# Optimization experiments

Measured on AMD Instinct MI355X. Metric: run time of the kernel, lower is better.

## Reference

```python
import jax, jax.numpy as jnp
import numpy as np

LN_EPS = 1e-5

def _layernorm(x, w, b):
    mu = jnp.mean(x, axis=-1, keepdims=True)
    var = jnp.mean((x - mu) ** 2, axis=-1, keepdims=True)
    return (x - mu) * jax.lax.rsqrt(var + LN_EPS) * w + b

def _parallel_scan(A, B, x):
    # A, B, x: (Bb, L, S). Log-space cumsum trick, faithful to torch version.
    A_safe = jnp.clip(A, 0.001, 0.999)
    log_A = jnp.log(A_safe + 1e-10)
    log_cum_A = jnp.cumsum(log_A, axis=1)
    log_cum_A_max = jnp.max(log_cum_A, axis=1, keepdims=True)
    log_cum_A_c = log_cum_A - log_cum_A_max
    cum_A = jnp.exp(log_cum_A_c)
    BX = B * x
    # shifted (exclusive) centered log-cumsum: zeros at t=0
    zeros = jnp.zeros_like(log_cum_A_c[:, :1])
    log_cum_shift = jnp.concatenate([zeros, log_cum_A_c[:, :-1]], axis=1)
    BX_norm = BX * jnp.exp(-log_cum_shift)
    cum_BX = jnp.cumsum(BX_norm, axis=1)
    return cum_BX * cum_A

def setup_inputs() -> dict:
    key = jax.random.key(0)
    ks = jax.random.split(key, 8)
    Bb, L, D, S = 16, 4096, 512, 64
    def xavier(k, shape, gain):
        fan_out, fan_in = shape
        std = gain * np.sqrt(2.0 / (fan_in + fan_out))
        return jax.random.normal(k, shape, jnp.float32) * std
    x = jax.random.normal(ks[0], (Bb, L, D), jnp.float32)
    Wx = xavier(ks[1], (S, D), 0.5)
    Wdt = xavier(ks[2], (S, D), 1.0)
    WB = xavier(ks[3], (S, D), 0.4)
    WC = xavier(ks[4], (S, D), 0.4)
    Wout = xavier(ks[5], (D, S), 0.5)
    # A_init = -rand*0.8 - 0.2 ; A_log = log(-A_init) = log(uniform(0.2, 1.0))
    A_log = jnp.log(jax.random.uniform(ks[6], (S,), jnp.float32, 0.2, 1.0))
    return {
        "x": x,
        "ln_w": jnp.ones((D,), jnp.float32),
        "ln_b": jnp.zeros((D,), jnp.float32),
        "Wx": Wx, "bx": jnp.zeros((S,), jnp.float32),
        "Wdt": Wdt, "bdt": jnp.zeros((S,), jnp.float32),
        "A_log": A_log,
        "WB": WB, "WC": WC,
        "Dp": jnp.zeros((D,), jnp.float32),
        "Wout": Wout, "bout": jnp.zeros((D,), jnp.float32),
    }

def reference(x, ln_w, ln_b, Wx, bx, Wdt, bdt, A_log, WB, WC, Dp, Wout, bout):
    x_norm = _layernorm(x, ln_w, ln_b)                       # (B,L,D)
    delta = jax.nn.softplus(x_norm @ Wdt.T + bdt) * 0.01 + 0.0001  # (B,L,S)
    B_t = x_norm @ WB.T                                      # (B,L,S)
    C_t = x_norm @ WC.T                                      # (B,L,S)
    A = -jnp.exp(A_log)                                      # (S,)
    x_proj = x_norm @ Wx.T + bx                              # (B,L,S)
    deltaA = jnp.clip(delta * A, -10.0, -0.0001)
    A_disc = jnp.exp(deltaA)
    B_disc = delta * B_t
    h = _parallel_scan(A_disc, B_disc, x_proj)               # (B,L,S)
    y = C_t * h
    y = jnp.where(jnp.any(~jnp.isfinite(y)), jnp.zeros_like(y), y)
    y = y @ Wout.T + bout                                    # (B,L,D)
    D_safe = jnp.clip(Dp, -2.0, 2.0)
    return y + D_safe * x
```

## Files before the change

### kernel.cpp

```cpp
#include <hip/hip_runtime.h>
#include <math.h>

typedef __attribute__((ext_vector_type(4))) float  floatx4;
typedef __attribute__((ext_vector_type(8))) short  shortx8;
typedef unsigned short ushort_t;
typedef unsigned int   uint32;

#define BB 16
#define LL 4096
#define DD 512
#define SS 64
#define NTOK (BB*LL)
#define NCH 64

__device__ __forceinline__ ushort_t f2bf(float f) {
    uint32 u = __float_as_uint(f);
    u += 0x7FFFu + ((u >> 16) & 1u);
    return (ushort_t)(u >> 16);
}

__global__ __launch_bounds__(256) void k_prep(
    const float* __restrict__ Wdt, const float* __restrict__ WB,
    const float* __restrict__ WC,  const float* __restrict__ Wx,
    const float* __restrict__ Wout,
    ushort_t* __restrict__ wcat, ushort_t* __restrict__ woutb)
{
    int tid = blockIdx.x * 256 + threadIdx.x;
    int n = tid >> 9, k = tid & 511;
    const float* src = (n < 64) ? Wdt : (n < 128) ? WB : (n < 192) ? WC : Wx;
    wcat[tid] = f2bf(src[(n & 63) * 512 + k]);
    if (tid < 512 * 64) woutb[tid] = f2bf(Wout[tid]);
}

__global__ __launch_bounds__(256) void k_ln_proj(
    const float* __restrict__ x, const float* __restrict__ lnw, const float* __restrict__ lnb,
    const ushort_t* __restrict__ wcat,
    const float* __restrict__ bdt, const float* __restrict__ bx_, const float* __restrict__ A_log,
    float* __restrict__ Ap, float* __restrict__ BXv, float* __restrict__ Ct,
    float* __restrict__ Asum, float* __restrict__ Bsum)
{
    __shared__ float sMean[64], sRstd[64];
    __shared__ __align__(16) char sBuf[46080];
    ushort_t* sA = (ushort_t*)sBuf;
    ushort_t* sB = sA + 64 * 72;
    float*    sPA = (float*)sBuf;
    float*    sPB = sPA + 64 * 17;

    const int tid  = threadIdx.x;
    const int wave = tid >> 6, lane = tid & 63;
    const int ln   = lane & 15, qd = lane >> 4;
    const int token0 = blockIdx.x * 64;

    for (int i = 0; i < 16; i++) {
        int tok = wave * 16 + i;
        const float4* xr = (const float4*)(x + (size_t)(token0 + tok) * DD);
        float4 a = xr[lane];
        float4 b = xr[64 + lane];
        float s = a.x + a.y + a.z + a.w + b.x + b.y + b.z + b.w;
        float q = a.x*a.x + a.y*a.y + a.z*a.z + a.w*a.w
                + b.x*b.x + b.y*b.y + b.z*b.z + b.w*b.w;
        #pragma unroll
        for (int off = 32; off > 0; off >>= 1) {
            s += __shfl_xor(s, off);
            q += __shfl_xor(q, off);
        }
        if (lane == 0) {
            float mu  = s * (1.0f / 512.0f);
            float var = q * (1.0f / 512.0f) - mu * mu;
            sMean[tok] = mu;
            sRstd[tok] = rsqrtf(var + 1e-5f);
        }
    }
    __syncthreads();

    floatx4 acc[4][4] = {};

    for (int kc = 0; kc < 8; kc++) {
        {
            int q = tid & 15, tr = tid >> 4;
            #pragma unroll
            for (int it = 0; it < 4; it++) {
                int tok = it * 16 + tr;
                float mu = sMean[tok], rs = sRstd[tok];
                float4 v  = *(const float4*)(x + (size_t)(token0 + tok) * DD + kc * 64 + q * 4);
                float4 w4 = *(const float4*)(lnw + kc * 64 + q * 4);
                float4 b4 = *(const float4*)(lnb + kc * 64 + q * 4);
                uint32 lo = (uint32)f2bf((v.x - mu) * rs * w4.x + b4.x)
                          | ((uint32)f2bf((v.y - mu) * rs * w4.y + b4.y) << 16);
                uint32 hi = (uint32)f2bf((v.z - mu) * rs * w4.z + b4.z)
                          | ((uint32)f2bf((v.w - mu) * rs * w4.w + b4.w) << 16);
                uint2 pk; pk.x = lo; pk.y = hi;
                *(uint2*)&sA[tok * 72 + q * 4] = pk;
            }
        }
        {
            #pragma unroll
            for (int it = 0; it < 8; it++) {
                int f = it * 256 + tid;
                int n = f >> 3, c8 = f & 7;
                uint4 v = *(const uint4*)(wcat + n * 512 + kc * 64 + c8 * 8);
                *(uint4*)&sB[n * 72 + c8 * 8] = v;
            }
        }
        __syncthreads();
        #pragma unroll
        for (int ks = 0; ks < 64; ks += 32) {
            shortx8 af[4], bf[4];
            #pragma unroll
            for (int mt = 0; mt < 4; mt++)
                af[mt] = *(const shortx8*)&sA[(mt * 16 + ln) * 72 + ks + qd * 8];
            #pragma unroll
            for (int nt = 0; nt < 4; nt++)
                bf[nt] = *(const shortx8*)&sB[(nt * 64 + wave * 16 + ln) * 72 + ks + qd * 8];
            #pragma unroll
            for (int mt = 0; mt < 4; mt++)
                #pragma unroll
                for (int nt = 0; nt < 4; nt++)
                    acc[mt][nt] = __builtin_amdgcn_mfma_f32_16x16x32_bf16(
                        af[mt], bf[nt], acc[mt][nt], 0, 0, 0);
        }
        __syncthreads();
    }

    {
        int s = wave * 16 + ln;
        float bdt_s = bdt[s], bx_s = bx_[s];
        float A_s = -expf(A_log[s]);
        bool fc = ((blockIdx.x & 63) == 0);
        #pragma unroll
        for (int mt = 0; mt < 4; mt++) {
            float Al = 1.f, Bl = 0.f;
            #pragma unroll
            for (int r = 0; r < 4; r++) {
                int tok = mt * 16 + qd * 4 + r;
                float zdt = acc[mt][0][r];
                float zb  = acc[mt][1][r];
                float zc  = acc[mt][2][r];
                float zx  = acc[mt][3][r];
                float zin = zdt + bdt_s;
                float sp  = fmaxf(zin, 0.0f) + log1pf(expf(-fabsf(zin)));
                float delta = sp * 0.01f + 1e-4f;
                float dA    = fminf(fmaxf(delta * A_s, -10.0f), -1e-4f);
                float Adisc = expf(dA);
                float a     = fminf(fmaxf(Adisc, 0.001f), 0.999f) + 1e-10f;
                float bxv   = delta * zb * (zx + bx_s);
                size_t g = (size_t)(token0 + tok) * 64 + s;
                Ap[g] = a; BXv[g] = bxv; Ct[g] = zc;
                bool first = fc && (tok == 0);
                float alpha = first ? 0.f : a;
                float beta  = first ? bxv : a * bxv;
                Al *= alpha;
                Bl = fmaf(alpha, Bl, beta);
            }
            sPA[s * 17 + mt * 4 + qd] = Al;
            sPB[s * 17 + mt * 4 + qd] = Bl;
        }
    }
    __syncthreads();
    if (tid < 64) {
        float A = sPA[tid * 17 + 0], B = sPB[tid * 17 + 0];
        #pragma unroll
        for (int g = 1; g < 16; g++) {
            float pa = sPA[tid * 17 + g], pb = sPB[tid * 17 + g];
            A *= pa;
            B = fmaf(pa, B, pb);
        }
        int o = blockIdx.x * 64 + tid;
        Asum[o] = A; Bsum[o] = B;
    }
}

__global__ __launch_bounds__(64) void k_scan_b(
    const float* __restrict__ Asum, const float* __restrict__ Bsum, float* __restrict__ Hin)
{
    int b = blockIdx.x, s = threadIdx.x;
    float h = 0.f;
    for (int tile = 0; tile < 4; tile++) {
        float rA[16], rB[16];
        #pragma unroll
        for (int cc = 0; cc < 16; cc++) {
            int o = (b * NCH + tile * 16 + cc) * 64 + s;
            rA[cc] = Asum[o]; rB[cc] = Bsum[o];
        }
        #pragma unroll
        for (int cc = 0; cc < 16; cc++) {
            int o = (b * NCH + tile * 16 + cc) * 64 + s;
            Hin[o] = h;
            h = fmaf(rA[cc], h, rB[cc]);
        }
    }
}

__global__ __launch_bounds__(512, 4) void k_out2(
    const float* __restrict__ Ap, const float* __restrict__ BXv, const float* __restrict__ Ct,
    const float* __restrict__ Hin, const ushort_t* __restrict__ woutb,
    const float* __restrict__ bout, const float* __restrict__ Dp,
    const float* __restrict__ x, float* __restrict__ out)
{
    __shared__ __align__(16) char buf[33024];
    ushort_t* sP   = (ushort_t*)buf;
    float*    sSA  = (float*)(buf + 9216);
    float*    sSB  = (float*)(buf + 9216 + 2048);
    float*    sOut = (float*)buf;

    const int tid  = threadIdx.x;
    const int wave = tid >> 6, lane = tid & 63;
    const int ln   = lane & 15, qd = lane >> 4;
    const int blk  = blockIdx.x;
    const int token0 = blk * 64;
    const bool fc = ((blk & 63) == 0);

    {
        const int s = lane, j = wave;
        size_t gbase = (size_t)token0 * 64 + (size_t)j * 8 * 64 + s;
        float av[8], vv[8];
        #pragma unroll
        for (int i = 0; i < 8; i++) {
            av[i] = Ap[gbase + (size_t)i * 64];
            vv[i] = BXv[gbase + (size_t)i * 64];
        }
        float Al = 1.f, Bl = 0.f;
        #pragma unroll
        for (int i = 0; i < 8; i++) {
            bool first = fc && (j == 0) && (i == 0);
            float alpha = first ? 0.f : av[i];
            float beta  = first ? vv[i] : av[i] * vv[i];
            Al *= alpha;
            Bl = fmaf(alpha, Bl, beta);
        }
        sSA[j * 64 + s] = Al;
        sSB[j * 64 + s] = Bl;
        __syncthreads();
        float h = Hin[blk * 64 + s];
        for (int jj = 0; jj < j; jj++)
            h = fmaf(sSA[jj * 64 + s], h, sSB[jj * 64 + s]);
        #pragma unroll
        for (int i = 0; i < 8; i++) {
            bool first = fc && (j == 0) && (i == 0);
            float alpha = first ? 0.f : av[i];
            float beta  = first ? vv[i] : av[i] * vv[i];
            h = fmaf(alpha, h, beta);
            float ct = Ct[gbase + (size_t)i * 64];
            sP[(j * 8 + i) * 72 + s] = f2bf(ct * h);
        }
    }
    __syncthreads();

    floatx4 acc[4][4] = {};
    const int d0 = wave * 64;
    #pragma unroll
    for (int ks = 0; ks < 64; ks += 32) {
        shortx8 af[4], bf[4];
        #pragma unroll
        for (int mt = 0; mt < 4; mt++)
            af[mt] = *(const shortx8*)&sP[(mt * 16 + ln) * 72 + ks + qd * 8];
        #pragma unroll
        for (int nt = 0; nt < 4; nt++)
            bf[nt] = *(const shortx8*)(woutb + (size_t)(d0 + nt * 16 + ln) * 64 + ks + qd * 8);
        #pragma unroll
        for (int mt = 0; mt < 4; mt++)
            #pragma unroll
            for (int nt = 0; nt < 4; nt++)
                acc[mt][nt] = __builtin_amdgcn_mfma_f32_16x16x32_bf16(
                    af[mt], bf[nt], acc[mt][nt], 0, 0, 0);
    }

    for (int mt = 0; mt < 4; mt++) {
        __syncthreads();
        #pragma unroll
        for (int nt = 0; nt < 4; nt++)
            #pragma unroll
            for (int r = 0; r < 4; r++)
                sOut[(qd * 4 + r) * 516 + d0 + nt * 16 + ln] = acc[mt][nt][r];
        __syncthreads();
        #pragma unroll
        for (int it = 0; it < 4; it++) {
            int idx = it * 512 + tid;
            int row = idx >> 7, c4 = (idx & 127) * 4;
            int tok = token0 + mt * 16 + row;
            float4 o  = *(float4*)&sOut[row * 516 + c4];
            float4 xv = *(const float4*)(x + (size_t)tok * DD + c4);
            float4 bo = *(const float4*)(bout + c4);
            float4 dp = *(const float4*)(Dp + c4);
            float4 res;
            res.x = fmaf(fminf(fmaxf(dp.x, -2.f), 2.f), xv.x, o.x + bo.x);
            res.y = fmaf(fminf(fmaxf(dp.y, -2.f), 2.f), xv.y, o.y + bo.y);
            res.z = fmaf(fminf(fmaxf(dp.z, -2.f), 2.f), xv.z, o.z + bo.z);
            res.w = fmaf(fminf(fmaxf(dp.w, -2.f), 2.f), xv.w, o.w + bo.w);
            *(float4*)(out + (size_t)tok * DD + c4) = res;
        }
    }
}

extern "C" void kernel_launch(void* const* d_in, const int* in_sizes, int n_in,
                              void* d_out, int out_size, void* d_ws, size_t ws_size,
                              hipStream_t stream)
{
    const float* x     = (const float*)d_in[0];
    const float* lnw   = (const float*)d_in[1];
    const float* lnb   = (const float*)d_in[2];
    const float* Wx    = (const float*)d_in[3];
    const float* bx_   = (const float*)d_in[4];
    const float* Wdt   = (const float*)d_in[5];
    const float* bdt   = (const float*)d_in[6];
    const float* A_log = (const float*)d_in[7];
    const float* WB    = (const float*)d_in[8];
    const float* WC    = (const float*)d_in[9];
    const float* Dp    = (const float*)d_in[10];
    const float* Wout  = (const float*)d_in[11];
    const float* bout  = (const float*)d_in[12];
    float* out = (float*)d_out;

    char* w = (char*)d_ws;
    constexpr size_t SZ_T = (size_t)NTOK * 64 * 4;
    float*    Ap    = (float*)(w);
    float*    BXv   = (float*)(w + SZ_T);
    float*    Ct    = (float*)(w + 2 * SZ_T);
    float*    Asum  = (float*)(w + 3 * SZ_T);
    float*    Bsum  = (float*)(w + 3 * SZ_T + 262144);
    float*    Hin   = (float*)(w + 3 * SZ_T + 2 * 262144);
    ushort_t* Wcat  = (ushort_t*)(w + 3 * SZ_T + 3 * 262144);
    ushort_t* WoutB = (ushort_t*)(w + 3 * SZ_T + 3 * 262144 + 262144);

    k_prep<<<512, 256, 0, stream>>>(Wdt, WB, WC, Wx, Wout, Wcat, WoutB);
    k_ln_proj<<<NTOK / 64, 256, 0, stream>>>(x, lnw, lnb, Wcat, bdt, bx_, A_log,
                                             Ap, BXv, Ct, Asum, Bsum);
    k_scan_b<<<BB, 64, 0, stream>>>(Asum, Bsum, Hin);
    k_out2<<<NTOK / 64, 512, 0, stream>>>(Ap, BXv, Ct, Hin, WoutB, bout, Dp, x, out);
}
```

Before: 341.7 us.

## Split LayerNorm into bf16 pass, use direct-to-LDS loads, restructure scan and output GEMM

LayerNorm now runs as its own kernel that writes a bf16 normalized activation buffer. The projection GEMM reads that buffer and the weights with global_load_lds into XOR-swizzled shared memory, using 128-token tiles across 8 waves. The serial per-batch scan is replaced by a wider kernel in which each block recomputes the chunk prefix from the chunk sums and writes C*h as bf16. The output GEMM is split across two blocks per token tile along D. In exchange, the normalized activations make an extra round trip through HBM and a bf16 intermediate buffer is added.

```diff
diff --git a/kernel.cpp b/kernel.cpp
--- a/kernel.cpp
+++ b/kernel.cpp
@@ -19,6 +19,12 @@
     return (ushort_t)(u >> 16);
 }
 
+__device__ __forceinline__ void gload16(const void* g, void* l) {
+    __builtin_amdgcn_global_load_lds(
+        (const __attribute__((address_space(1))) unsigned int*)g,
+        (__attribute__((address_space(3))) unsigned int*)l, 16, 0, 0);
+}
+
 __global__ __launch_bounds__(256) void k_prep(
     const float* __restrict__ Wdt, const float* __restrict__ WB,
     const float* __restrict__ WC,  const float* __restrict__ Wx,
@@ -32,86 +38,84 @@
     if (tid < 512 * 64) woutb[tid] = f2bf(Wout[tid]);
 }
 
-__global__ __launch_bounds__(256) void k_ln_proj(
+__global__ __launch_bounds__(256) void k_ln(
     const float* __restrict__ x, const float* __restrict__ lnw, const float* __restrict__ lnb,
-    const ushort_t* __restrict__ wcat,
+    ushort_t* __restrict__ xn)
+{
+    const int wave = threadIdx.x >> 6, lane = threadIdx.x & 63;
+    const int tok = blockIdx.x * 4 + wave;
+    const float4* xr = (const float4*)(x + (size_t)tok * DD);
+    float4 a = xr[lane * 2], b = xr[lane * 2 + 1];
+    float s = a.x + a.y + a.z + a.w + b.x + b.y + b.z + b.w;
+    float q = a.x*a.x + a.y*a.y + a.z*a.z + a.w*a.w
+            + b.x*b.x + b.y*b.y + b.z*b.z + b.w*b.w;
+    #pragma unroll
+    for (int off = 32; off > 0; off >>= 1) {
+        s += __shfl_xor(s, off);
+        q += __shfl_xor(q, off);
+    }
+    float mu = s * (1.0f / 512.0f);
+    float rs = rsqrtf(q * (1.0f / 512.0f) - mu * mu + 1e-5f);
+    float4 wa = ((const float4*)lnw)[lane * 2], wb = ((const float4*)lnw)[lane * 2 + 1];
+    float4 ba = ((const float4*)lnb)[lane * 2], bb = ((const float4*)lnb)[lane * 2 + 1];
+    uint4 pk;
+    pk.x = (uint32)f2bf((a.x - mu) * rs * wa.x + ba.x) | ((uint32)f2bf((a.y - mu) * rs * wa.y + ba.y) << 16);
+    pk.y = (uint32)f2bf((a.z - mu) * rs * wa.z + ba.z) | ((uint32)f2bf((a.w - mu) * rs * wa.w + ba.w) << 16);
+    pk.z = (uint32)f2bf((b.x - mu) * rs * wb.x + bb.x) | ((uint32)f2bf((b.y - mu) * rs * wb.y + bb.y) << 16);
+    pk.w = (uint32)f2bf((b.z - mu) * rs * wb.z + bb.z) | ((uint32)f2bf((b.w - mu) * rs * wb.w + bb.w) << 16);
+    ((uint4*)(xn + (size_t)tok * DD))[lane] = pk;
+}
+
+__global__ __launch_bounds__(512, 4) void k_proj(
+    const ushort_t* __restrict__ xn, const ushort_t* __restrict__ wcat,
     const float* __restrict__ bdt, const float* __restrict__ bx_, const float* __restrict__ A_log,
     float* __restrict__ Ap, float* __restrict__ BXv, float* __restrict__ Ct,
     float* __restrict__ Asum, float* __restrict__ Bsum)
 {
-    __shared__ float sMean[64], sRstd[64];
-    __shared__ __align__(16) char sBuf[46080];
+    __shared__ __align__(16) char sBuf[49152];
     ushort_t* sA = (ushort_t*)sBuf;
-    ushort_t* sB = sA + 64 * 72;
+    ushort_t* sB = (ushort_t*)(sBuf + 16384);
     float*    sPA = (float*)sBuf;
-    float*    sPB = sPA + 64 * 17;
+    float*    sPB = sPA + 2 * 64 * 17;
 
     const int tid  = threadIdx.x;
     const int wave = tid >> 6, lane = tid & 63;
     const int ln   = lane & 15, qd = lane >> 4;
-    const int token0 = blockIdx.x * 64;
-
-    for (int i = 0; i < 16; i++) {
-        int tok = wave * 16 + i;
-        const float4* xr = (const float4*)(x + (size_t)(token0 + tok) * DD);
-        float4 a = xr[lane];
-        float4 b = xr[64 + lane];
-        float s = a.x + a.y + a.z + a.w + b.x + b.y + b.z + b.w;
-        float q = a.x*a.x + a.y*a.y + a.z*a.z + a.w*a.w
-                + b.x*b.x + b.y*b.y + b.z*b.z + b.w*b.w;
-        #pragma unroll
-        for (int off = 32; off > 0; off >>= 1) {
-            s += __shfl_xor(s, off);
-            q += __shfl_xor(q, off);
-        }
-        if (lane == 0) {
-            float mu  = s * (1.0f / 512.0f);
-            float var = q * (1.0f / 512.0f) - mu * mu;
-            sMean[tok] = mu;
-            sRstd[tok] = rsqrtf(var + 1e-5f);
-        }
-    }
-    __syncthreads();
+    const int mh   = wave >> 2, nq = wave & 3;
+    const int token0 = blockIdx.x * 128;
+
+    int tA[2], cA[2], tB[4], cB[4];
+    #pragma unroll
+    for (int r = 0; r < 2; r++) { int sl = r * 512 + tid; tA[r] = sl >> 3; cA[r] = ((sl & 7) ^ (tA[r] & 7)) * 8; }
+    #pragma unroll
+    for (int r = 0; r < 4; r++) { int sl = r * 512 + tid; tB[r] = sl >> 3; cB[r] = ((sl & 7) ^ (tB[r] & 7)) * 8; }
 
     floatx4 acc[4][4] = {};
 
     for (int kc = 0; kc < 8; kc++) {
-        {
-            int q = tid & 15, tr = tid >> 4;
-            #pragma unroll
-            for (int it = 0; it < 4; it++) {
-                int tok = it * 16 + tr;
-                float mu = sMean[tok], rs = sRstd[tok];
-                float4 v  = *(const float4*)(x + (size_t)(token0 + tok) * DD + kc * 64 + q * 4);
-                float4 w4 = *(const float4*)(lnw + kc * 64 + q * 4);
-                float4 b4 = *(const float4*)(lnb + kc * 64 + q * 4);
-                uint32 lo = (uint32)f2bf((v.x - mu) * rs * w4.x + b4.x)
-                          | ((uint32)f2bf((v.y - mu) * rs * w4.y + b4.y) << 16);
-                uint32 hi = (uint32)f2bf((v.z - mu) * rs * w4.z + b4.z)
-                          | ((uint32)f2bf((v.w - mu) * rs * w4.w + b4.w) << 16);
-                uint2 pk; pk.x = lo; pk.y = hi;
-                *(uint2*)&sA[tok * 72 + q * 4] = pk;
+        const int kb = kc * 64;
+        #pragma unroll
+        for (int r = 0; r < 2; r++)
+            gload16(xn + (size_t)(token0 + tA[r]) * DD + kb + cA[r],
+                    sBuf + r * 8192 + wave * 1024);
+        #pragma unroll
+        for (int r = 0; r < 4; r++)
+            gload16(wcat + (size_t)tB[r] * DD + kb + cB[r],
+                    sBuf + 16384 + r * 8192 + wave * 1024);
+        __syncthreads();
+        #pragma unroll
+        for (int ks8 = 0; ks8 < 8; ks8 += 4) {
+            shortx8 af[4], bf[4];
+            #pragma unroll
+            for (int mt = 0; mt < 4; mt++) {
+                int t = mh * 64 + mt * 16 + ln;
+                af[mt] = *(const shortx8*)&sA[t * 64 + (((ks8 + qd) ^ (ln & 7)) << 3)];
             }
-        }
-        {
-            #pragma unroll
-            for (int it = 0; it < 8; it++) {
-                int f = it * 256 + tid;
-                int n = f >> 3, c8 = f & 7;
-                uint4 v = *(const uint4*)(wcat + n * 512 + kc * 64 + c8 * 8);
-                *(uint4*)&sB[n * 72 + c8 * 8] = v;
+            #pragma unroll
+            for (int nt = 0; nt < 4; nt++) {
+                int n = nt * 64 + nq * 16 + ln;
+                bf[nt] = *(const shortx8*)&sB[n * 64 + (((ks8 + qd) ^ (ln & 7)) << 3)];
             }
-        }
-        __syncthreads();
-        #pragma unroll
-        for (int ks = 0; ks < 64; ks += 32) {
-            shortx8 af[4], bf[4];
-            #pragma unroll
-            for (int mt = 0; mt < 4; mt++)
-                af[mt] = *(const shortx8*)&sA[(mt * 16 + ln) * 72 + ks + qd * 8];
-            #pragma unroll
-            for (int nt = 0; nt < 4; nt++)
-                bf[nt] = *(const shortx8*)&sB[(nt * 64 + wave * 16 + ln) * 72 + ks + qd * 8];
             #pragma unroll
             for (int mt = 0; mt < 4; mt++)
                 #pragma unroll
@@ -123,16 +127,17 @@
     }
 
     {
-        int s = wave * 16 + ln;
+        const int s = nq * 16 + ln;
         float bdt_s = bdt[s], bx_s = bx_[s];
         float A_s = -expf(A_log[s]);
-        bool fc = ((blockIdx.x & 63) == 0);
+        const bool fc = ((blockIdx.x & 31) == 0) && (mh == 0);
         #pragma unroll
         for (int mt = 0; mt < 4; mt++) {
             float Al = 1.f, Bl = 0.f;
             #pragma unroll
             for (int r = 0; r < 4; r++) {
-                int tok = mt * 16 + qd * 4 + r;
+                int tl  = mt * 16 + qd * 4 + r;
+                int tok = token0 + mh * 64 + tl;
                 float zdt = acc[mt][0][r];
                 float zb  = acc[mt][1][r];
                 float zc  = acc[mt][2][r];
@@ -141,122 +146,108 @@
                 float sp  = fmaxf(zin, 0.0f) + log1pf(expf(-fabsf(zin)));
                 float delta = sp * 0.01f + 1e-4f;
                 float dA    = fminf(fmaxf(delta * A_s, -10.0f), -1e-4f);
-                float Adisc = expf(dA);
-                float a     = fminf(fmaxf(Adisc, 0.001f), 0.999f) + 1e-10f;
+                float a     = fminf(fmaxf(expf(dA), 0.001f), 0.999f) + 1e-10f;
                 float bxv   = delta * zb * (zx + bx_s);
-                size_t g = (size_t)(token0 + tok) * 64 + s;
+                size_t g = (size_t)tok * 64 + s;
                 Ap[g] = a; BXv[g] = bxv; Ct[g] = zc;
-                bool first = fc && (tok == 0);
+                bool first = fc && (tl == 0);
                 float alpha = first ? 0.f : a;
                 float beta  = first ? bxv : a * bxv;
                 Al *= alpha;
                 Bl = fmaf(alpha, Bl, beta);
             }
-            sPA[s * 17 + mt * 4 + qd] = Al;
-            sPB[s * 17 + mt * 4 + qd] = Bl;
+            sPA[(mh * 64 + s) * 17 + mt * 4 + qd] = Al;
+            sPB[(mh * 64 + s) * 17 + mt * 4 + qd] = Bl;
         }
     }
     __syncthreads();
-    if (tid < 64) {
-        float A = sPA[tid * 17 + 0], B = sPB[tid * 17 + 0];
+    if (tid < 128) {
+        int ch = tid >> 6, ss = tid & 63;
+        const float* pa = &sPA[(ch * 64 + ss) * 17];
+        const float* pb = &sPB[(ch * 64 + ss) * 17];
+        float A = pa[0], B = pb[0];
         #pragma unroll
         for (int g = 1; g < 16; g++) {
-            float pa = sPA[tid * 17 + g], pb = sPB[tid * 17 + g];
-            A *= pa;
-            B = fmaf(pa, B, pb);
-        }
-        int o = blockIdx.x * 64 + tid;
+            A *= pa[g];
+            B = fmaf(pa[g], B, pb[g]);
+        }
+        int o = (blockIdx.x * 2 + ch) * 64 + ss;
         Asum[o] = A; Bsum[o] = B;
     }
 }
 
-__global__ __launch_bounds__(64) void k_scan_b(
-    const float* __restrict__ Asum, const float* __restrict__ Bsum, float* __restrict__ Hin)
-{
-    int b = blockIdx.x, s = threadIdx.x;
+__global__ __launch_bounds__(256) void k_scan(
+    const float* __restrict__ Ap, const float* __restrict__ BXv, const float* __restrict__ Ct,
+    const float* __restrict__ Asum, const float* __restrict__ Bsum,
+    ushort_t* __restrict__ P)
+{
+    __shared__ float sAs[4096], sBs[4096];
+    const int tid = threadIdx.x;
+    const int b = blockIdx.x >> 4, cq = blockIdx.x & 15;
+    #pragma unroll
+    for (int i = 0; i < 16; i++) {
+        int idx = i * 256 + tid;
+        sAs[idx] = Asum[b * 4096 + idx];
+        sBs[idx] = Bsum[b * 4096 + idx];
+    }
+    __syncthreads();
+    const int w = tid >> 6, s = tid & 63;
+    const int c = cq * 4 + w;
     float h = 0.f;
-    for (int tile = 0; tile < 4; tile++) {
-        float rA[16], rB[16];
-        #pragma unroll
-        for (int cc = 0; cc < 16; cc++) {
-            int o = (b * NCH + tile * 16 + cc) * 64 + s;
-            rA[cc] = Asum[o]; rB[cc] = Bsum[o];
-        }
-        #pragma unroll
-        for (int cc = 0; cc < 16; cc++) {
-            int o = (b * NCH + tile * 16 + cc) * 64 + s;
-            Hin[o] = h;
-            h = fmaf(rA[cc], h, rB[cc]);
-        }
-    }
-}
-
-__global__ __launch_bounds__(512, 4) void k_out2(
-    const float* __restrict__ Ap, const float* __restrict__ BXv, const float* __restrict__ Ct,
-    const float* __restrict__ Hin, const ushort_t* __restrict__ woutb,
+    for (int cc = 0; cc < c; cc++)
+        h = fmaf(sAs[cc * 64 + s], h, sBs[cc * 64 + s]);
+    size_t base = ((size_t)b * LL + c * 64) * 64 + s;
+    const bool fc = (c == 0);
+    #pragma unroll 8
+    for (int t = 0; t < 64; t++) {
+        float a = Ap[base + (size_t)t * 64];
+        float v = BXv[base + (size_t)t * 64];
+        float alpha = (fc && t == 0) ? 0.f : a;
+        float beta  = (fc && t == 0) ? v   : a * v;
+        h = fmaf(alpha, h, beta);
+        P[base + (size_t)t * 64] = f2bf(Ct[base + (size_t)t * 64] * h);
+    }
+}
+
+__global__ __launch_bounds__(256, 4) void k_gemm2(
+    const ushort_t* __restrict__ P, const ushort_t* __restrict__ woutb,
     const float* __restrict__ bout, const float* __restrict__ Dp,
     const float* __restrict__ x, float* __restrict__ out)
 {
-    __shared__ __align__(16) char buf[33024];
-    ushort_t* sP   = (ushort_t*)buf;
-    float*    sSA  = (float*)(buf + 9216);
-    float*    sSB  = (float*)(buf + 9216 + 2048);
-    float*    sOut = (float*)buf;
+    __shared__ __align__(16) char sBuf2[16640];
+    ushort_t* sP   = (ushort_t*)sBuf2;
+    float*    sOut = (float*)sBuf2;
 
     const int tid  = threadIdx.x;
     const int wave = tid >> 6, lane = tid & 63;
     const int ln   = lane & 15, qd = lane >> 4;
-    const int blk  = blockIdx.x;
-    const int token0 = blk * 64;
-    const bool fc = ((blk & 63) == 0);
-
-    {
-        const int s = lane, j = wave;
-        size_t gbase = (size_t)token0 * 64 + (size_t)j * 8 * 64 + s;
-        float av[8], vv[8];
-        #pragma unroll
-        for (int i = 0; i < 8; i++) {
-            av[i] = Ap[gbase + (size_t)i * 64];
-            vv[i] = BXv[gbase + (size_t)i * 64];
-        }
-        float Al = 1.f, Bl = 0.f;
-        #pragma unroll
-        for (int i = 0; i < 8; i++) {
-            bool first = fc && (j == 0) && (i == 0);
-            float alpha = first ? 0.f : av[i];
-            float beta  = first ? vv[i] : av[i] * vv[i];
-            Al *= alpha;
-            Bl = fmaf(alpha, Bl, beta);
-        }
-        sSA[j * 64 + s] = Al;
-        sSB[j * 64 + s] = Bl;
-        __syncthreads();
-        float h = Hin[blk * 64 + s];
-        for (int jj = 0; jj < j; jj++)
-            h = fmaf(sSA[jj * 64 + s], h, sSB[jj * 64 + s]);
-        #pragma unroll
-        for (int i = 0; i < 8; i++) {
-            bool first = fc && (j == 0) && (i == 0);
-            float alpha = first ? 0.f : av[i];
-            float beta  = first ? vv[i] : av[i] * vv[i];
-            h = fmaf(alpha, h, beta);
-            float ct = Ct[gbase + (size_t)i * 64];
-            sP[(j * 8 + i) * 72 + s] = f2bf(ct * h);
-        }
+    const int nq   = wave;
+    const int token0 = (blockIdx.x >> 1) * 64;
+    const int nh = (blockIdx.x & 1) * 256;
+
+    #pragma unroll
+    for (int r = 0; r < 2; r++) {
+        int sl = r * 256 + tid;
+        int t = sl >> 3, k8 = (sl & 7) ^ (t & 7);
+        gload16(P + (size_t)(token0 + t) * 64 + k8 * 8,
+                sBuf2 + r * 4096 + wave * 1024);
     }
     __syncthreads();
 
     floatx4 acc[4][4] = {};
-    const int d0 = wave * 64;
-    #pragma unroll
-    for (int ks = 0; ks < 64; ks += 32) {
+    #pragma unroll
+    for (int ks8 = 0; ks8 < 8; ks8 += 4) {
         shortx8 af[4], bf[4];
         #pragma unroll
-        for (int mt = 0; mt < 4; mt++)
-            af[mt] = *(const shortx8*)&sP[(mt * 16 + ln) * 72 + ks + qd * 8];
-        #pragma unroll
-        for (int nt = 0; nt < 4; nt++)
-            bf[nt] = *(const shortx8*)(woutb + (size_t)(d0 + nt * 16 + ln) * 64 + ks + qd * 8);
+        for (int mt = 0; mt < 4; mt++) {
+            int t = mt * 16 + ln;
+            af[mt] = *(const shortx8*)&sP[t * 64 + (((ks8 + qd) ^ (ln & 7)) << 3)];
+        }
+        #pragma unroll
+        for (int nt = 0; nt < 4; nt++) {
+            int d = nh + nq * 64 + nt * 16 + ln;
+            bf[nt] = *(const shortx8*)(woutb + (size_t)d * 64 + (ks8 + qd) * 8);
+        }
         #pragma unroll
         for (int mt = 0; mt < 4; mt++)
             #pragma unroll
@@ -271,23 +262,24 @@
         for (int nt = 0; nt < 4; nt++)
             #pragma unroll
             for (int r = 0; r < 4; r++)
-                sOut[(qd * 4 + r) * 516 + d0 + nt * 16 + ln] = acc[mt][nt][r];
+                sOut[(qd * 4 + r) * 260 + nq * 64 + nt * 16 + ln] = acc[mt][nt][r];
         __syncthreads();
         #pragma unroll
-        for (int it = 0; it < 4; it++) {
-            int idx = it * 512 + tid;
-            int row = idx >> 7, c4 = (idx & 127) * 4;
+        for (int i = 0; i < 4; i++) {
+            int idx = i * 256 + tid;
+            int row = idx >> 6, c4 = (idx & 63) * 4;
             int tok = token0 + mt * 16 + row;
-            float4 o  = *(float4*)&sOut[row * 516 + c4];
-            float4 xv = *(const float4*)(x + (size_t)tok * DD + c4);
-            float4 bo = *(const float4*)(bout + c4);
-            float4 dp = *(const float4*)(Dp + c4);
+            int d   = nh + c4;
+            float4 o  = *(float4*)&sOut[row * 260 + c4];
+            float4 xv = *(const float4*)(x + (size_t)tok * DD + d);
+            float4 bo = *(const float4*)(bout + d);
+            float4 dp = *(const float4*)(Dp + d);
             float4 res;
             res.x = fmaf(fminf(fmaxf(dp.x, -2.f), 2.f), xv.x, o.x + bo.x);
             res.y = fmaf(fminf(fmaxf(dp.y, -2.f), 2.f), xv.y, o.y + bo.y);
             res.z = fmaf(fminf(fmaxf(dp.z, -2.f), 2.f), xv.z, o.z + bo.z);
             res.w = fmaf(fminf(fmaxf(dp.w, -2.f), 2.f), xv.w, o.w + bo.w);
-            *(float4*)(out + (size_t)tok * DD + c4) = res;
+            *(float4*)(out + (size_t)tok * DD + d) = res;
         }
     }
 }
@@ -312,19 +304,22 @@
     float* out = (float*)d_out;
 
     char* w = (char*)d_ws;
-    constexpr size_t SZ_T = (size_t)NTOK * 64 * 4;
-    float*    Ap    = (float*)(w);
-    float*    BXv   = (float*)(w + SZ_T);
-    float*    Ct    = (float*)(w + 2 * SZ_T);
-    float*    Asum  = (float*)(w + 3 * SZ_T);
-    float*    Bsum  = (float*)(w + 3 * SZ_T + 262144);
-    float*    Hin   = (float*)(w + 3 * SZ_T + 2 * 262144);
-    ushort_t* Wcat  = (ushort_t*)(w + 3 * SZ_T + 3 * 262144);
-    ushort_t* WoutB = (ushort_t*)(w + 3 * SZ_T + 3 * 262144 + 262144);
+    constexpr size_t SZ_XN = (size_t)NTOK * DD * 2;
+    constexpr size_t SZ_T  = (size_t)NTOK * 64 * 4;
+    ushort_t* xn    = (ushort_t*)(w);
+    ushort_t* Pm    = (ushort_t*)(w);
+    float*    Ap    = (float*)(w + SZ_XN);
+    float*    BXv   = (float*)(w + SZ_XN + SZ_T);
+    float*    Ct    = (float*)(w + SZ_XN + 2 * SZ_T);
+    float*    Asum  = (float*)(w + SZ_XN + 3 * SZ_T);
+    float*    Bsum  = (float*)(w + SZ_XN + 3 * SZ_T + 262144);
+    ushort_t* Wcat  = (ushort_t*)(w + SZ_XN + 3 * SZ_T + 2 * 262144);
+    ushort_t* WoutB = (ushort_t*)(w + SZ_XN + 3 * SZ_T + 2 * 262144 + 262144);
 
     k_prep<<<512, 256, 0, stream>>>(Wdt, WB, WC, Wx, Wout, Wcat, WoutB);
-    k_ln_proj<<<NTOK / 64, 256, 0, stream>>>(x, lnw, lnb, Wcat, bdt, bx_, A_log,
-                                             Ap, BXv, Ct, Asum, Bsum);
-    k_scan_b<<<BB, 64, 0, stream>>>(Asum, Bsum, Hin);
-    k_out2<<<NTOK / 64, 512, 0, stream>>>(Ap, BXv, Ct, Hin, WoutB, bout, Dp, x, out);
-}
+    k_ln<<<NTOK / 4, 256, 0, stream>>>(x, lnw, lnb, xn);
+    k_proj<<<NTOK / 128, 512, 0, stream>>>(xn, Wcat, bdt, bx_, A_log,
+                                           Ap, BXv, Ct, Asum, Bsum);
+    k_scan<<<BB * 16, 256, 0, stream>>>(Ap, BXv, Ct, Asum, Bsum, Pm);
+    k_gemm2<<<(NTOK / 64) * 2, 256, 0, stream>>>(Pm, WoutB, bout, Dp, x, out);
+}
```

New measurement: 337.5 us. No clear change (-1.2%).
